# Performance work log

Hardware: AMD Instinct MI355X
Metric: run time of the kernel (lower is better)

## Reference

```python
import jax, jax.numpy as jnp
import numpy as np

B, N, HID, H, M = 4, 16384, 512, 8, 32
D = HID // H  # 64


def setup_inputs() -> dict:
    key = jax.random.key(0)
    ks = jax.random.split(key, 8)
    s = 0.02
    return {
        "x": jax.random.normal(ks[0], (B, N, HID), jnp.float32),
        "wkv": jax.random.normal(ks[1], (2 * HID, HID), jnp.float32) * s,
        "bkv": jnp.zeros((2 * HID,), jnp.float32),
        "wtq": jax.random.normal(ks[2], (H, M, D), jnp.float32) * s,
        "alpha1": jnp.ones((H,), jnp.float32),
        "mix1_w": jax.random.normal(ks[3], (H * M, H * M), jnp.float32) * (1.0 / np.sqrt(H * M)),
        "ln1_w": jnp.ones((D,), jnp.float32),
        "ln1_b": jnp.zeros((D,), jnp.float32),
        "wqkv": jax.random.normal(ks[4], (3 * HID, HID), jnp.float32) * s,
        "wout": jax.random.normal(ks[5], (HID, HID), jnp.float32) * s,
        "bout": jnp.zeros((HID,), jnp.float32),
    }


def _layernorm(x, w, b, eps=1e-5):
    mu = x.mean(-1, keepdims=True)
    var = ((x - mu) ** 2).mean(-1, keepdims=True)
    return (x - mu) * jax.lax.rsqrt(var + eps) * w + b


def reference(x, wkv, bkv, wtq, alpha1, mix1_w, ln1_w, ln1_b, wqkv, wout, bout):
    # key/value projection: [B, N, 2*HID]
    kv = x @ wkv.T + bkv
    xk, xv = jnp.split(kv, 2, axis=-1)
    xk = xk.reshape(B, N, H, D).transpose(0, 2, 1, 3)  # b h n d
    xv = xv.reshape(B, N, H, D).transpose(0, 2, 1, 3)
    # slice scores + 1x1 conv head-mixing over the (H*M) channel dim
    scores = jnp.einsum('hmd,bhnd->bhmn', wtq, xk)
    scores = jnp.einsum('oc,bcn->bon', mix1_w, scores.reshape(B, H * M, N)).reshape(B, H, M, N)
    # softmax over the slice dim M (dim=-2)
    sw = jax.nn.softmax(scores * alpha1[:, None, None], axis=-2)  # b h m n
    # weighted reduction to slice tokens, normalized by total weight per slice
    tok = jnp.einsum('bhmn,bhnd->bhmd', sw, xv)
    tok = tok / (sw.sum(axis=-1, keepdims=True) + 1e-5)
    tok = _layernorm(tok, ln1_w, ln1_b)
    tok = tok.transpose(0, 2, 1, 3).reshape(B, M, HID)  # b m (h d)
    # small inner MHA over the M=32 slice tokens
    qkv = tok @ wqkv.T
    q, k, v = jnp.split(qkv, 3, axis=-1)
    q = q.reshape(B, M, H, D).transpose(0, 2, 1, 3)
    k = k.reshape(B, M, H, D).transpose(0, 2, 1, 3)
    v = v.reshape(B, M, H, D).transpose(0, 2, 1, 3)
    dots = jnp.einsum('bhqd,bhkd->bhqk', q, k) * (D ** -0.5)
    attn = jax.nn.softmax(dots, axis=-1)
    out_tok = jnp.einsum('bhqk,bhkd->bhqd', attn, v)
    # broadcast slice tokens back to the N points via slice weights
    out = jnp.einsum('bhmd,bhmn->bhnd', out_tok, sw)
    out = out.transpose(0, 2, 1, 3).reshape(B, N, HID)
    out = out @ wout.T + bout
    return (out, sw, alpha1[:, None, None], jnp.zeros((H, M), jnp.float32), attn)
```

## Files before the change

### kernel.cpp

```cpp
#include <hip/hip_runtime.h>
#include <hip/hip_bf16.h>

#define B_ 4
#define N_ 16384
#define HID_ 512
#define H_ 8
#define M_ 32
#define D_ 64
#define HM_ 256

typedef __hip_bfloat16 bf16;
typedef __bf16 bf16x8 __attribute__((ext_vector_type(8)));
typedef float f32x4 __attribute__((ext_vector_type(4)));

__device__ __forceinline__ void gl_lds16(const bf16* g, bf16* l) {
    __builtin_amdgcn_global_load_lds(
        (const __attribute__((address_space(1))) void*)g,
        (__attribute__((address_space(3))) void*)l, 16, 0, 0);
}

__device__ __forceinline__ int xcd_swz(int lin, int nwg) {
    return (lin & 7) * (nwg >> 3) + (lin >> 3);
}

__device__ __forceinline__ void stage_tile_lin(const bf16* __restrict__ G, long long r0,
        int kk, int ld, bf16* lds, int t) {
    const int l = t & 63, w = t >> 6;
    const int srow = l >> 3;
    const int skel = (l & 7) * 8;
#pragma unroll
    for (int j = 0; j < 4; ++j) {
        int q = j * 4 + w;
        gl_lds16(G + (r0 + q * 8 + srow) * (long long)ld + kk + skel, lds + q * 512);
    }
}

__device__ __forceinline__ void mfma_core(
        const bf16* __restrict__ Ag, const bf16* __restrict__ Bg,
        long long arow0, int bcol0, int lda, int ldb, int kiters,
        bf16* As, bf16* Bs, f32x4 acc[4][4]) {
    const int t = threadIdx.x;
    const int l = t & 63, w = t >> 6;
    const int wm = w >> 1, wn = w & 1;
    for (int kt = 0; kt < kiters; ++kt) {
        const int kk = kt * 64;
        stage_tile_lin(Ag, arow0, kk, lda, As, t);
        stage_tile_lin(Bg, bcol0, kk, ldb, Bs, t);
        __syncthreads();
#pragma unroll
        for (int ks = 0; ks < 64; ks += 32) {
            bf16x8 af[4], bfr[4];
#pragma unroll
            for (int mf = 0; mf < 4; ++mf)
                af[mf] = *(const bf16x8*)(As + (wm * 64 + mf * 16 + (l & 15)) * 64 + ks + (l >> 4) * 8);
#pragma unroll
            for (int nf = 0; nf < 4; ++nf)
                bfr[nf] = *(const bf16x8*)(Bs + (wn * 64 + nf * 16 + (l & 15)) * 64 + ks + (l >> 4) * 8);
#pragma unroll
            for (int mf = 0; mf < 4; ++mf)
#pragma unroll
                for (int nf = 0; nf < 4; ++nf)
                    acc[mf][nf] = __builtin_amdgcn_mfma_f32_16x16x32_bf16(af[mf], bfr[nf], acc[mf][nf], 0, 0, 0);
        }
        __syncthreads();
    }
}

__global__ __launch_bounds__(256) void k_cast4(const float* __restrict__ s,
        ushort* __restrict__ d) {
    long long i = (long long)blockIdx.x * 256 + threadIdx.x;
    float4 v = reinterpret_cast<const float4*>(s)[i];
    ushort4 o;
    bf16 a0 = __float2bfloat16(v.x), a1 = __float2bfloat16(v.y);
    bf16 a2 = __float2bfloat16(v.z), a3 = __float2bfloat16(v.w);
    o.x = *(ushort*)&a0; o.y = *(ushort*)&a1; o.z = *(ushort*)&a2; o.w = *(ushort*)&a3;
    reinterpret_cast<ushort4*>(d)[i] = o;
}

__global__ __launch_bounds__(256) void k_wfused(const float* __restrict__ mix1,
        const float* __restrict__ wtq, float* __restrict__ wf) {
    const int idx = blockIdx.x * 256 + threadIdx.x;
    const int o = idx >> 9, k = idx & 511;
    const int h = k >> 6, dd = k & 63;
    float s = 0.f;
#pragma unroll
    for (int m = 0; m < 32; ++m)
        s += mix1[(long long)o * 256 + h * 32 + m] * wtq[((long long)h * 32 + m) * 64 + dd];
    wf[(long long)o * 512 + k] = s;
}

__global__ __launch_bounds__(256) void k_wsc(const float* __restrict__ wf,
        const float* __restrict__ wkv, const float* __restrict__ bkv,
        const float* __restrict__ alpha1, bf16* __restrict__ wv_sc,
        float* __restrict__ bias768) {
    __shared__ float wfrow[512];
    __shared__ float red[256];
    const int o = blockIdx.x, t = threadIdx.x;
    wfrow[t] = wf[(long long)o * 512 + t];
    wfrow[t + 256] = wf[(long long)o * 512 + 256 + t];
    __syncthreads();
    const float al = alpha1[o >> 5];
    float a0 = 0.f, a1 = 0.f;
    for (int c = 0; c < 512; ++c) {
        float wv = wfrow[c];
        a0 += wv * wkv[(long long)c * 512 + t];
        a1 += wv * wkv[(long long)c * 512 + t + 256];
    }
    wv_sc[(long long)(512 + o) * 512 + t] = __float2bfloat16(a0 * al);
    wv_sc[(long long)(512 + o) * 512 + t + 256] = __float2bfloat16(a1 * al);
    float p = wfrow[t] * bkv[t] + wfrow[t + 256] * bkv[t + 256];
    red[t] = p; __syncthreads();
    for (int s = 128; s >= 1; s >>= 1) {
        if (t < s) red[t] += red[t + s];
        __syncthreads();
    }
    if (t == 0) bias768[512 + o] = red[0] * al;
}

__global__ __launch_bounds__(256) void k_prep(const float* __restrict__ bkv,
        float* __restrict__ bias768) {
    int j = blockIdx.x * 256 + threadIdx.x;
    bias768[j] = bkv[512 + j];
}

__global__ __launch_bounds__(256) void k12_mfma(const bf16* __restrict__ xb,
        const bf16* __restrict__ wv_sc, const float* __restrict__ bias768,
        bf16* __restrict__ xv, bf16* __restrict__ sc) {
    __shared__ bf16 As[128 * 64], Bs[128 * 64];
    f32x4 acc[4][4];
#pragma unroll
    for (int i = 0; i < 4; ++i)
#pragma unroll
        for (int j = 0; j < 4; ++j) acc[i][j] = (f32x4)(0.0f);
    const int wg = xcd_swz(blockIdx.y * 6 + blockIdx.x, 3072);
    const int bx = wg % 6, by = wg / 6;
    const long long arow0 = (long long)by * 128;
    const int bcol0 = bx * 128;
    mfma_core(xb, wv_sc, arow0, bcol0, 512, 512, 8, As, Bs, acc);
    const int l = threadIdx.x & 63, w = threadIdx.x >> 6;
    const int wm = w >> 1, wn = w & 1;
#pragma unroll
    for (int mf = 0; mf < 4; ++mf) {
#pragma unroll
        for (int nf = 0; nf < 4; ++nf) {
            int col = bcol0 + wn * 64 + nf * 16 + (l & 15);
            float bv = bias768[col];
#pragma unroll
            for (int r = 0; r < 4; ++r) {
                long long row = arow0 + wm * 64 + mf * 16 + (l >> 4) * 4 + r;
                bf16 hv = __float2bfloat16(acc[mf][nf][r] + bv);
                if (col < 512) xv[row * 512 + col] = hv;
                else           sc[row * 256 + (col - 512)] = hv;
            }
        }
    }
}

__global__ __launch_bounds__(256) void k_softmax(const bf16* __restrict__ sc,
        float* __restrict__ swout, bf16* __restrict__ sw_bt,
        float* __restrict__ part) {
    __shared__ float T[32][257];
    const int t = threadIdx.x;
    const int b = blockIdx.y;
    const int n0 = blockIdx.x * 32;
    const long long rb = (long long)b * N_ + n0;
    for (int i = 0; i < 32; ++i)
        T[i][t] = __bfloat162float(sc[(rb + i) * 256 + t]);
    __syncthreads();
    const int nl = t & 31, h = t >> 5;
    float v[32];
    float mx = -1e30f;
#pragma unroll
    for (int i = 0; i < 32; ++i) { v[i] = T[nl][h * 32 + i]; mx = fmaxf(mx, v[i]); }
    float sum = 0.f;
#pragma unroll
    for (int i = 0; i < 32; ++i) { v[i] = __expf(v[i] - mx); sum += v[i]; }
    float rinv = 1.f / sum;
#pragma unroll
    for (int i = 0; i < 32; ++i) T[nl][h * 32 + i] = v[i] * rinv;
    __syncthreads();
#pragma unroll
    for (int jo = 0; jo < 32; ++jo) {
        int o = h * 32 + jo;
        swout[((long long)b * HM_ + o) * N_ + n0 + nl] = T[nl][o];
    }
    for (int i = 0; i < 32; ++i)
        sw_bt[(rb + i) * 256 + t] = __float2bfloat16(T[i][t]);
    float s = 0.f;
#pragma unroll
    for (int i = 0; i < 32; ++i) s += T[i][t];
    part[((long long)b * 512 + blockIdx.x) * 256 + t] = s;
}

__global__ __launch_bounds__(256) void k_swsum2(const float* __restrict__ part,
        float* __restrict__ swsum) {
    const int b = blockIdx.x, c = threadIdx.x;
    float s = 0.f;
    for (int nb = 0; nb < 512; ++nb)
        s += part[((long long)b * 512 + nb) * 256 + c];
    swsum[b * 256 + c] = s;
}

__global__ __launch_bounds__(256) void k3_tok(const float* __restrict__ sw,
        const bf16* __restrict__ xv, float* __restrict__ tok_part) {
    __shared__ __align__(16) float smem[17408];
    float (*swsT)[36] = reinterpret_cast<float(*)[36]>(smem);
    bf16* xvs = reinterpret_cast<bf16*>(smem + 9216);
    const int t = threadIdx.x;
    const int chunk = blockIdx.x;
    const int bh = blockIdx.y;
    const int n0 = chunk * 256;
    const int b = bh >> 3, h = bh & 7;
    const long long swbase = ((long long)bh * 32) * N_ + n0;
#pragma unroll
    for (int p = 0; p < 8; ++p) {
        float4 v;
        v.x = sw[swbase + (long long)(p * 4 + 0) * N_ + t];
        v.y = sw[swbase + (long long)(p * 4 + 1) * N_ + t];
        v.z = sw[swbase + (long long)(p * 4 + 2) * N_ + t];
        v.w = sw[swbase + (long long)(p * 4 + 3) * N_ + t];
        *reinterpret_cast<float4*>(&swsT[t][p * 4]) = v;
    }
    {
        const uint* xg = reinterpret_cast<const uint*>(xv + ((long long)b * N_ + n0) * 512 + h * 64);
        uint* xls = reinterpret_cast<uint*>(xvs);
#pragma unroll
        for (int p = 0; p < 32; ++p) {
            int idx = p * 256 + t;
            int nl = idx >> 5, prt = idx & 31;
            xls[nl * 32 + prt] = xg[(long long)nl * 256 + prt];
        }
    }
    __syncthreads();
    const int l = t & 63, w = t >> 6;
    const int nlh = l >> 5, mtile = (l >> 3) & 3, dtile = l & 7;
    const int m0 = mtile * 8, d0 = dtile * 8;
    float acc[8][8] = {};
    const int wbase = w * 64;
    for (int i = 0; i < 32; ++i) {
        int nl = wbase + i * 2 + nlh;
        float4 s0 = *reinterpret_cast<const float4*>(&swsT[nl][m0]);
        float4 s1 = *reinterpret_cast<const float4*>(&swsT[nl][m0 + 4]);
        uint4 xi = *reinterpret_cast<const uint4*>(&xvs[nl * 64 + d0]);
        float xvf[8];
        xvf[0] = __uint_as_float(xi.x << 16); xvf[1] = __uint_as_float(xi.x & 0xffff0000u);
        xvf[2] = __uint_as_float(xi.y << 16); xvf[3] = __uint_as_float(xi.y & 0xffff0000u);
        xvf[4] = __uint_as_float(xi.z << 16); xvf[5] = __uint_as_float(xi.z & 0xffff0000u);
        xvf[6] = __uint_as_float(xi.w << 16); xvf[7] = __uint_as_float(xi.w & 0xffff0000u);
        float sm[8] = {s0.x, s0.y, s0.z, s0.w, s1.x, s1.y, s1.z, s1.w};
#pragma unroll
        for (int mi = 0; mi < 8; ++mi)
#pragma unroll
            for (int di = 0; di < 8; ++di)
                acc[mi][di] += sm[mi] * xvf[di];
    }
    __syncthreads();
    float* red = smem;
    float* rb = red + (w * 2 + nlh) * 2048;
#pragma unroll
    for (int mi = 0; mi < 8; ++mi) {
        float4 lo = {acc[mi][0], acc[mi][1], acc[mi][2], acc[mi][3]};
        float4 hi = {acc[mi][4], acc[mi][5], acc[mi][6], acc[mi][7]};
        *reinterpret_cast<float4*>(&rb[(m0 + mi) * 64 + d0]) = lo;
        *reinterpret_cast<float4*>(&rb[(m0 + mi) * 64 + d0 + 4]) = hi;
    }
    __syncthreads();
#pragma unroll
    for (int pp = 0; pp < 2; ++pp) {
        int idx4 = pp * 1024 + t * 4;
        float4 s = {0.f, 0.f, 0.f, 0.f};
#pragma unroll
        for (int r = 0; r < 8; ++r) {
            float4 v = *reinterpret_cast<const float4*>(&red[r * 2048 + idx4]);
            s.x += v.x; s.y += v.y; s.z += v.z; s.w += v.w;
        }
        *reinterpret_cast<float4*>(&tok_part[((long long)bh * 64 + chunk) * 2048 + idx4]) = s;
    }
}

__global__ __launch_bounds__(64) void k4a_ln(const float* __restrict__ tok_part,
        const float* __restrict__ swsum, const float* __restrict__ ln_w,
        const float* __restrict__ ln_b, float* __restrict__ tok_ln) {
    const int bid = blockIdx.x;
    const int bh = bid >> 5, m = bid & 31;
    const int d = threadIdx.x;
    float s = 0.f;
    for (int ch = 0; ch < 64; ++ch)
        s += tok_part[(((long long)bh * 64 + ch) * 32 + m) * 64 + d];
    float tokv = s / (swsum[bid] + 1e-5f);
    float mu = tokv;
#pragma unroll
    for (int mk = 32; mk >= 1; mk >>= 1) mu += __shfl_xor(mu, mk, 64);
    mu *= (1.f / 64.f);
    float df = tokv - mu;
    float var = df * df;
#pragma unroll
    for (int mk = 32; mk >= 1; mk >>= 1) var += __shfl_xor(var, mk, 64);
    var *= (1.f / 64.f);
    float y = df * rsqrtf(var + 1e-5f) * ln_w[d] + ln_b[d];
    const int b = bh >> 3, h = bh & 7;
    tok_ln[((long long)b * 32 + m) * 512 + h * 64 + d] = y;
}

__global__ __launch_bounds__(256) void k_wqT(const float* __restrict__ wq,
        float* __restrict__ wqT) {
    __shared__ float tile[32][33];
    const int k0 = blockIdx.x * 32;
    const int j0 = blockIdx.y * 32;
    const int tx = threadIdx.x & 31, ty = threadIdx.x >> 5;
#pragma unroll
    for (int r = 0; r < 32; r += 8)
        tile[ty + r][tx] = wq[(long long)(j0 + ty + r) * 512 + k0 + tx];
    __syncthreads();
#pragma unroll
    for (int r = 0; r < 32; r += 8)
        wqT[(long long)(k0 + ty + r) * 1536 + j0 + tx] = tile[tx][ty + r];
}

__global__ __launch_bounds__(256) void k4b_qkv(const float* __restrict__ tok_ln,
        const float* __restrict__ wqT, float* __restrict__ qkv) {
    const int j = (blockIdx.x % 6) * 256 + threadIdx.x;
    const int r0 = (blockIdx.x / 6) * 4;
    float a0 = 0, a1 = 0, a2 = 0, a3 = 0;
    for (int k = 0; k < 512; ++k) {
        float wv = wqT[(long long)k * 1536 + j];
        a0 += tok_ln[(r0 + 0) * 512 + k] * wv;
        a1 += tok_ln[(r0 + 1) * 512 + k] * wv;
        a2 += tok_ln[(r0 + 2) * 512 + k] * wv;
        a3 += tok_ln[(r0 + 3) * 512 + k] * wv;
    }
    qkv[(long long)(r0 + 0) * 1536 + j] = a0;
    qkv[(long long)(r0 + 1) * 1536 + j] = a1;
    qkv[(long long)(r0 + 2) * 1536 + j] = a2;
    qkv[(long long)(r0 + 3) * 1536 + j] = a3;
}

__global__ __launch_bounds__(256) void k4c_attn(const float* __restrict__ qkv,
        float* __restrict__ out_tok, float* __restrict__ attn_out) {
    __shared__ float qsT[64][33], ksT[64][33], vsT[64][33];
    __shared__ float att[32][33];
    __shared__ float rinv[32];
    const int t = threadIdx.x;
    const int bid = blockIdx.x;
    const int b = bid >> 3, h = bid & 7;
#pragma unroll
    for (int i = 0; i < 8; ++i) {
        int idx = i * 256 + t;
        int mi = idx >> 6, dd = idx & 63;
        long long base = ((long long)b * 32 + mi) * 1536 + h * 64 + dd;
        qsT[dd][mi] = qkv[base];
        ksT[dd][mi] = qkv[base + 512];
        vsT[dd][mi] = qkv[base + 1024];
    }
    __syncthreads();
#pragma unroll
    for (int i = 0; i < 4; ++i) {
        int idx = i * 256 + t;
        int qi = idx >> 5, ki = idx & 31;
        float s = 0.f;
#pragma unroll
        for (int dd = 0; dd < 64; ++dd) s += qsT[dd][qi] * ksT[dd][ki];
        att[qi][ki] = s * 0.125f;
    }
    __syncthreads();
    if (t < 32) {
        float mx = -1e30f;
        for (int k = 0; k < 32; ++k) mx = fmaxf(mx, att[t][k]);
        float sum = 0.f;
        for (int k = 0; k < 32; ++k) { float e = __expf(att[t][k] - mx); att[t][k] = e; sum += e; }
        rinv[t] = 1.f / sum;
    }
    __syncthreads();
#pragma unroll
    for (int i = 0; i < 4; ++i) {
        int idx = i * 256 + t;
        int qi = idx >> 5, ki = idx & 31;
        float a = att[qi][ki] * rinv[qi];
        att[qi][ki] = a;
        attn_out[(long long)bid * 1024 + qi * 32 + ki] = a;
    }
    __syncthreads();
#pragma unroll
    for (int i = 0; i < 8; ++i) {
        int idx = i * 256 + t;
        int qi = idx >> 6, dd = idx & 63;
        float s = 0.f;
#pragma unroll
        for (int ki = 0; ki < 32; ++ki) s += att[qi][ki] * vsT[dd][ki];
        out_tok[((long long)bid * 32 + qi) * 64 + dd] = s;
    }
}

__global__ __launch_bounds__(256) void k5_w2(const float* __restrict__ wout,
        const float* __restrict__ out_tok, bf16* __restrict__ W2) {
    const int bid = blockIdx.x;
    const int b = bid >> 9, o = bid & 511;
    const int t = threadIdx.x;
    const int h = t >> 5, m = t & 31;
    float s = 0.f;
#pragma unroll
    for (int dd = 0; dd < 64; ++dd)
        s += wout[(long long)o * 512 + h * 64 + dd]
           * out_tok[(((long long)b * 8 + h) * 32 + m) * 64 + dd];
    W2[(long long)bid * 256 + t] = __float2bfloat16(s);
}

__global__ __launch_bounds__(256) void k6_mfma(const bf16* __restrict__ sw_bt,
        const bf16* __restrict__ W2, const float* __restrict__ bout,
        float* __restrict__ out) {
    __shared__ bf16 As[128 * 64], Bs[128 * 64];
    f32x4 acc[4][4];
#pragma unroll
    for (int i = 0; i < 4; ++i)
#pragma unroll
        for (int j = 0; j < 4; ++j) acc[i][j] = (f32x4)(0.0f);
    const int wg = xcd_swz((blockIdx.z * 128 + blockIdx.y) * 4 + blockIdx.x, 2048);
    const int bx = wg & 3, by = (wg >> 2) & 127, bz = wg >> 9;
    const long long arow0 = (long long)by * 128;
    const int bcol0 = bx * 128;
    mfma_core(sw_bt + (long long)bz * N_ * 256, W2 + (long long)bz * 512 * 256,
              arow0, bcol0, 256, 256, 4, As, Bs, acc);
    const int l = threadIdx.x & 63, w = threadIdx.x >> 6;
    const int wm = w >> 1, wn = w & 1;
#pragma unroll
    for (int mf = 0; mf < 4; ++mf) {
#pragma unroll
        for (int nf = 0; nf < 4; ++nf) {
            int col = bcol0 + wn * 64 + nf * 16 + (l & 15);
            float bv = bout[col];
#pragma unroll
            for (int r = 0; r < 4; ++r) {
                long long row = arow0 + wm * 64 + mf * 16 + (l >> 4) * 4 + r;
                out[((long long)bz * N_ + row) * 512 + col] = acc[mf][nf][r] + bv;
            }
        }
    }
}

__global__ void k_misc(const float* __restrict__ alpha1,
        float* __restrict__ outA, float* __restrict__ outZ) {
    int t = threadIdx.x;
    if (t < 8) outA[t] = alpha1[t];
    outZ[t] = 0.f;
}

extern "C" void kernel_launch(void* const* d_in, const int* in_sizes, int n_in,
                              void* d_out, int out_size, void* d_ws, size_t ws_size,
                              hipStream_t stream) {
    const float* x      = (const float*)d_in[0];
    const float* wkv    = (const float*)d_in[1];
    const float* bkv    = (const float*)d_in[2];
    const float* wtq    = (const float*)d_in[3];
    const float* alpha1 = (const float*)d_in[4];
    const float* mix1_w = (const float*)d_in[5];
    const float* ln1_w  = (const float*)d_in[6];
    const float* ln1_b  = (const float*)d_in[7];
    const float* wqkv   = (const float*)d_in[8];
    const float* wout   = (const float*)d_in[9];
    const float* bout   = (const float*)d_in[10];

    float* out    = (float*)d_out;
    float* swout  = out + 33554432LL;
    float* alphaO = out + 50331648LL;
    float* zerosO = out + 50331656LL;
    float* attnO  = out + 50331912LL;

    char* ws = (char*)d_ws;
    bf16*  xb        = (bf16*)(ws);
    float* wqkvT     = (float*)(ws);
    float* swsum_prt = (float*)(ws + 33554432LL);
    float* wf_f32    = (float*)(ws + 35651584LL);
    bf16*  sc        = (bf16*)(ws + 67108864LL);
    bf16*  sw_bt     = (bf16*)(ws + 100663296LL);
    bf16*  xv        = (bf16*)(ws + 134217728LL);
    float* tok_part  = (float*)(ws + 201326592LL);
    float* swsum     = (float*)(ws + 218103808LL);
    float* tok_ln    = (float*)(ws + 218107904LL);
    float* qkv       = (float*)(ws + 218370048LL);
    float* out_tok   = (float*)(ws + 219156480LL);
    bf16*  W2b       = (bf16*)(ws + 219418624LL);
    bf16*  wv_sc     = (bf16*)(ws + 220467200LL);
    float* bias768   = (float*)(ws + 221253632LL);

    k_cast4<<<256, 256, 0, stream>>>(wkv + 262144, (ushort*)wv_sc);
    k_wfused<<<512, 256, 0, stream>>>(mix1_w, wtq, wf_f32);
    k_wsc<<<256, 256, 0, stream>>>(wf_f32, wkv, bkv, alpha1, wv_sc, bias768);
    k_prep<<<2, 256, 0, stream>>>(bkv, bias768);
    k_cast4<<<32768, 256, 0, stream>>>(x, (ushort*)xb);
    k12_mfma<<<dim3(6, 512), 256, 0, stream>>>(xb, wv_sc, bias768, xv, sc);
    k_softmax<<<dim3(512, 4), 256, 0, stream>>>(sc, swout, sw_bt, swsum_prt);
    k_wqT<<<dim3(16, 48), 256, 0, stream>>>(wqkv, wqkvT);
    k_swsum2<<<4, 256, 0, stream>>>(swsum_prt, swsum);
    k3_tok<<<dim3(64, 32), 256, 0, stream>>>(swout, xv, tok_part);
    k4a_ln<<<1024, 64, 0, stream>>>(tok_part, swsum, ln1_w, ln1_b, tok_ln);
    k4b_qkv<<<192, 256, 0, stream>>>(tok_ln, wqkvT, qkv);
    k4c_attn<<<32, 256, 0, stream>>>(qkv, out_tok, attnO);
    k5_w2<<<2048, 256, 0, stream>>>(wout, out_tok, W2b);
    k6_mfma<<<dim3(4, 128, 4), 256, 0, stream>>>(sw_bt, W2b, bout, out);
    k_misc<<<1, 256, 0, stream>>>(alpha1, alphaO, zerosO);
}
```

Baseline: 364.1 us.

## Fuse slice softmax and column sums into projection GEMM epilogue

Moves the softmax over the slice dimension into the k12 GEMM epilogue, using wave shuffles across 16-lane groups. It also writes sw (fp32 transposed) and sw_bt (bf16) directly from registers through an LDS staging tile. This removes the bf16 score round-trip through memory and the separate k_softmax and k_swsum2 launches. Per-tile column sums are written as partials and reduced inside k4a_ln, and k3_tok now reads the compact bf16 sw_bt instead of fp32 sw. The softmax epilogue adds register and shuffle work to the GEMM, and k3_tok now uses bf16-rounded weights.

```diff
diff --git a/kernel.cpp b/kernel.cpp
--- a/kernel.cpp
+++ b/kernel.cpp
@@ -21,6 +21,11 @@
 
 __device__ __forceinline__ int xcd_swz(int lin, int nwg) {
     return (lin & 7) * (nwg >> 3) + (lin >> 3);
+}
+
+__device__ __forceinline__ uint bpk(float lo, float hi) {
+    bf16 a = __float2bfloat16(lo), b = __float2bfloat16(hi);
+    return (uint)(*(ushort*)&a) | ((uint)(*(ushort*)&b) << 16);
 }
 
 __device__ __forceinline__ void stage_tile_lin(const bf16* __restrict__ G, long long r0,
@@ -125,8 +130,11 @@
 
 __global__ __launch_bounds__(256) void k12_mfma(const bf16* __restrict__ xb,
         const bf16* __restrict__ wv_sc, const float* __restrict__ bias768,
-        bf16* __restrict__ xv, bf16* __restrict__ sc) {
-    __shared__ bf16 As[128 * 64], Bs[128 * 64];
+        bf16* __restrict__ xv, float* __restrict__ swout,
+        bf16* __restrict__ sw_bt, float* __restrict__ part) {
+    __shared__ __align__(16) bf16 smem[16384];
+    bf16* As = smem;
+    bf16* Bs = smem + 8192;
     f32x4 acc[4][4];
 #pragma unroll
     for (int i = 0; i < 4; ++i)
@@ -137,71 +145,118 @@
     const long long arow0 = (long long)by * 128;
     const int bcol0 = bx * 128;
     mfma_core(xb, wv_sc, arow0, bcol0, 512, 512, 8, As, Bs, acc);
-    const int l = threadIdx.x & 63, w = threadIdx.x >> 6;
-    const int wm = w >> 1, wn = w & 1;
-#pragma unroll
-    for (int mf = 0; mf < 4; ++mf) {
-#pragma unroll
-        for (int nf = 0; nf < 4; ++nf) {
-            int col = bcol0 + wn * 64 + nf * 16 + (l & 15);
-            float bv = bias768[col];
-#pragma unroll
-            for (int r = 0; r < 4; ++r) {
-                long long row = arow0 + wm * 64 + mf * 16 + (l >> 4) * 4 + r;
-                bf16 hv = __float2bfloat16(acc[mf][nf][r] + bv);
-                if (col < 512) xv[row * 512 + col] = hv;
-                else           sc[row * 256 + (col - 512)] = hv;
+
+    const int t = threadIdx.x;
+    const int l = t & 63, w = t >> 6, wm = w >> 1, wn = w & 1;
+    const int l15 = l & 15, lq = l >> 4;
+#pragma unroll
+    for (int nf = 0; nf < 4; ++nf) {
+        float bv = bias768[bcol0 + wn * 64 + nf * 16 + l15];
+#pragma unroll
+        for (int mf = 0; mf < 4; ++mf)
+#pragma unroll
+            for (int r = 0; r < 4; ++r) acc[mf][nf][r] += bv;
+    }
+    float* eps = (float*)smem;
+    float* my = eps + w * 1088;
+
+    if (bcol0 >= 512) {
+#pragma unroll
+        for (int mf = 0; mf < 4; ++mf)
+#pragma unroll
+            for (int r = 0; r < 4; ++r)
+#pragma unroll
+                for (int g = 0; g < 2; ++g) {
+                    float v0 = acc[mf][2 * g][r], v1 = acc[mf][2 * g + 1][r];
+                    float mx = fmaxf(v0, v1);
+#pragma unroll
+                    for (int mk = 1; mk <= 8; mk <<= 1) mx = fmaxf(mx, __shfl_xor(mx, mk));
+                    float e0 = __expf(v0 - mx), e1 = __expf(v1 - mx);
+                    float s = e0 + e1;
+#pragma unroll
+                    for (int mk = 1; mk <= 8; mk <<= 1) s += __shfl_xor(s, mk);
+                    float ri = 1.f / s;
+                    acc[mf][2 * g][r] = e0 * ri;
+                    acc[mf][2 * g + 1][r] = e1 * ri;
+                }
+        {
+            float* cpart = eps + 4352;
+#pragma unroll
+            for (int nf = 0; nf < 4; ++nf) {
+                float ps = 0.f;
+#pragma unroll
+                for (int mf = 0; mf < 4; ++mf)
+#pragma unroll
+                    for (int r = 0; r < 4; ++r) ps += acc[mf][nf][r];
+                ps += __shfl_xor(ps, 16);
+                ps += __shfl_xor(ps, 32);
+                if (lq == 0) cpart[wm * 128 + wn * 64 + nf * 16 + l15] = ps;
             }
-        }
-    }
-}
-
-__global__ __launch_bounds__(256) void k_softmax(const bf16* __restrict__ sc,
-        float* __restrict__ swout, bf16* __restrict__ sw_bt,
-        float* __restrict__ part) {
-    __shared__ float T[32][257];
-    const int t = threadIdx.x;
-    const int b = blockIdx.y;
-    const int n0 = blockIdx.x * 32;
-    const long long rb = (long long)b * N_ + n0;
-    for (int i = 0; i < 32; ++i)
-        T[i][t] = __bfloat162float(sc[(rb + i) * 256 + t]);
-    __syncthreads();
-    const int nl = t & 31, h = t >> 5;
-    float v[32];
-    float mx = -1e30f;
-#pragma unroll
-    for (int i = 0; i < 32; ++i) { v[i] = T[nl][h * 32 + i]; mx = fmaxf(mx, v[i]); }
-    float sum = 0.f;
-#pragma unroll
-    for (int i = 0; i < 32; ++i) { v[i] = __expf(v[i] - mx); sum += v[i]; }
-    float rinv = 1.f / sum;
-#pragma unroll
-    for (int i = 0; i < 32; ++i) T[nl][h * 32 + i] = v[i] * rinv;
-    __syncthreads();
-#pragma unroll
-    for (int jo = 0; jo < 32; ++jo) {
-        int o = h * 32 + jo;
-        swout[((long long)b * HM_ + o) * N_ + n0 + nl] = T[nl][o];
-    }
-    for (int i = 0; i < 32; ++i)
-        sw_bt[(rb + i) * 256 + t] = __float2bfloat16(T[i][t]);
-    float s = 0.f;
-#pragma unroll
-    for (int i = 0; i < 32; ++i) s += T[i][t];
-    part[((long long)b * 512 + blockIdx.x) * 256 + t] = s;
-}
-
-__global__ __launch_bounds__(256) void k_swsum2(const float* __restrict__ part,
-        float* __restrict__ swsum) {
-    const int b = blockIdx.x, c = threadIdx.x;
-    float s = 0.f;
-    for (int nb = 0; nb < 512; ++nb)
-        s += part[((long long)b * 512 + nb) * 256 + c];
-    swsum[b * 256 + c] = s;
-}
-
-__global__ __launch_bounds__(256) void k3_tok(const float* __restrict__ sw,
+            __syncthreads();
+            if (t < 128)
+                part[(long long)by * 256 + (bcol0 - 512) + t] = cpart[t] + cpart[128 + t];
+            __syncthreads();
+        }
+        const int b = (int)(arow0 >> 14);
+        const int nloc = (int)(arow0 & 16383) + wm * 64;
+#pragma unroll
+        for (int mf = 0; mf < 4; ++mf) {
+#pragma unroll
+            for (int nf = 0; nf < 4; ++nf)
+#pragma unroll
+                for (int r = 0; r < 4; ++r)
+                    my[(lq * 4 + r) * 68 + nf * 16 + l15] = acc[mf][nf][r];
+#pragma unroll
+            for (int p = 0; p < 2; ++p) {
+                int lrow = p * 8 + (l >> 3);
+                const float* src = my + lrow * 68 + (l & 7) * 8;
+                float4 v0 = *(const float4*)src, v1 = *(const float4*)(src + 4);
+                uint4 pk;
+                pk.x = bpk(v0.x, v0.y); pk.y = bpk(v0.z, v0.w);
+                pk.z = bpk(v1.x, v1.y); pk.w = bpk(v1.z, v1.w);
+                long long grow = arow0 + wm * 64 + mf * 16 + lrow;
+                int gcol = (bcol0 - 512) + wn * 64 + (l & 7) * 8;
+                *reinterpret_cast<uint4*>(sw_bt + grow * 256 + gcol) = pk;
+            }
+            {
+                int cglob = (bcol0 - 512) + wn * 64 + l;
+                float* dst = swout + ((long long)b * HM_ + cglob) * N_ + nloc + mf * 16;
+#pragma unroll
+                for (int r4 = 0; r4 < 4; ++r4) {
+                    float4 v;
+                    v.x = my[(r4 * 4 + 0) * 68 + l];
+                    v.y = my[(r4 * 4 + 1) * 68 + l];
+                    v.z = my[(r4 * 4 + 2) * 68 + l];
+                    v.w = my[(r4 * 4 + 3) * 68 + l];
+                    *reinterpret_cast<float4*>(dst + r4 * 4) = v;
+                }
+            }
+        }
+    } else {
+#pragma unroll
+        for (int mf = 0; mf < 4; ++mf) {
+#pragma unroll
+            for (int nf = 0; nf < 4; ++nf)
+#pragma unroll
+                for (int r = 0; r < 4; ++r)
+                    my[(lq * 4 + r) * 68 + nf * 16 + l15] = acc[mf][nf][r];
+#pragma unroll
+            for (int p = 0; p < 2; ++p) {
+                int lrow = p * 8 + (l >> 3);
+                const float* src = my + lrow * 68 + (l & 7) * 8;
+                float4 v0 = *(const float4*)src, v1 = *(const float4*)(src + 4);
+                uint4 pk;
+                pk.x = bpk(v0.x, v0.y); pk.y = bpk(v0.z, v0.w);
+                pk.z = bpk(v1.x, v1.y); pk.w = bpk(v1.z, v1.w);
+                long long grow = arow0 + wm * 64 + mf * 16 + lrow;
+                int gcol = bcol0 + wn * 64 + (l & 7) * 8;
+                *reinterpret_cast<uint4*>(xv + grow * 512 + gcol) = pk;
+            }
+        }
+    }
+}
+
+__global__ __launch_bounds__(256) void k3_tok(const bf16* __restrict__ sw_bt,
         const bf16* __restrict__ xv, float* __restrict__ tok_part) {
     __shared__ __align__(16) float smem[17408];
     float (*swsT)[36] = reinterpret_cast<float(*)[36]>(smem);
@@ -211,15 +266,17 @@
     const int bh = blockIdx.y;
     const int n0 = chunk * 256;
     const int b = bh >> 3, h = bh & 7;
-    const long long swbase = ((long long)bh * 32) * N_ + n0;
-#pragma unroll
-    for (int p = 0; p < 8; ++p) {
-        float4 v;
-        v.x = sw[swbase + (long long)(p * 4 + 0) * N_ + t];
-        v.y = sw[swbase + (long long)(p * 4 + 1) * N_ + t];
-        v.z = sw[swbase + (long long)(p * 4 + 2) * N_ + t];
-        v.w = sw[swbase + (long long)(p * 4 + 3) * N_ + t];
-        *reinterpret_cast<float4*>(&swsT[t][p * 4]) = v;
+    {
+        const long long base = ((long long)(b * N_ + n0 + t)) * 256 + h * 32;
+        const uint4* sp = reinterpret_cast<const uint4*>(sw_bt + base);
+        uint4 qs[4] = {sp[0], sp[1], sp[2], sp[3]};
+        const uint* qu = reinterpret_cast<const uint*>(qs);
+#pragma unroll
+        for (int j = 0; j < 16; ++j) {
+            uint u = qu[j];
+            swsT[t][2 * j] = __uint_as_float(u << 16);
+            swsT[t][2 * j + 1] = __uint_as_float(u & 0xffff0000u);
+        }
     }
     {
         const uint* xg = reinterpret_cast<const uint*>(xv + ((long long)b * N_ + n0) * 512 + h * 64);
@@ -279,7 +336,7 @@
 }
 
 __global__ __launch_bounds__(64) void k4a_ln(const float* __restrict__ tok_part,
-        const float* __restrict__ swsum, const float* __restrict__ ln_w,
+        const float* __restrict__ part, const float* __restrict__ ln_w,
         const float* __restrict__ ln_b, float* __restrict__ tok_ln) {
     const int bid = blockIdx.x;
     const int bh = bid >> 5, m = bid & 31;
@@ -287,7 +344,12 @@
     float s = 0.f;
     for (int ch = 0; ch < 64; ++ch)
         s += tok_part[(((long long)bh * 64 + ch) * 32 + m) * 64 + d];
-    float tokv = s / (swsum[bid] + 1e-5f);
+    const int b = bid >> 8, c = bid & 255;
+    float ssum = part[((long long)(b * 128 + d)) * 256 + c]
+               + part[((long long)(b * 128 + 64 + d)) * 256 + c];
+#pragma unroll
+    for (int mk = 32; mk >= 1; mk >>= 1) ssum += __shfl_xor(ssum, mk, 64);
+    float tokv = s / (ssum + 1e-5f);
     float mu = tokv;
 #pragma unroll
     for (int mk = 32; mk >= 1; mk >>= 1) mu += __shfl_xor(mu, mk, 64);
@@ -298,8 +360,8 @@
     for (int mk = 32; mk >= 1; mk >>= 1) var += __shfl_xor(var, mk, 64);
     var *= (1.f / 64.f);
     float y = df * rsqrtf(var + 1e-5f) * ln_w[d] + ln_b[d];
-    const int b = bh >> 3, h = bh & 7;
-    tok_ln[((long long)b * 32 + m) * 512 + h * 64 + d] = y;
+    const int bb = bh >> 3, h = bh & 7;
+    tok_ln[((long long)bb * 32 + m) * 512 + h * 64 + d] = y;
 }
 
 __global__ __launch_bounds__(256) void k_wqT(const float* __restrict__ wq,
@@ -468,13 +530,11 @@
     char* ws = (char*)d_ws;
     bf16*  xb        = (bf16*)(ws);
     float* wqkvT     = (float*)(ws);
-    float* swsum_prt = (float*)(ws + 33554432LL);
     float* wf_f32    = (float*)(ws + 35651584LL);
-    bf16*  sc        = (bf16*)(ws + 67108864LL);
+    float* part      = (float*)(ws + 67108864LL);
     bf16*  sw_bt     = (bf16*)(ws + 100663296LL);
     bf16*  xv        = (bf16*)(ws + 134217728LL);
     float* tok_part  = (float*)(ws + 201326592LL);
-    float* swsum     = (float*)(ws + 218103808LL);
     float* tok_ln    = (float*)(ws + 218107904LL);
     float* qkv       = (float*)(ws + 218370048LL);
     float* out_tok   = (float*)(ws + 219156480LL);
@@ -487,12 +547,10 @@
     k_wsc<<<256, 256, 0, stream>>>(wf_f32, wkv, bkv, alpha1, wv_sc, bias768);
     k_prep<<<2, 256, 0, stream>>>(bkv, bias768);
     k_cast4<<<32768, 256, 0, stream>>>(x, (ushort*)xb);
-    k12_mfma<<<dim3(6, 512), 256, 0, stream>>>(xb, wv_sc, bias768, xv, sc);
-    k_softmax<<<dim3(512, 4), 256, 0, stream>>>(sc, swout, sw_bt, swsum_prt);
+    k12_mfma<<<dim3(6, 512), 256, 0, stream>>>(xb, wv_sc, bias768, xv, swout, sw_bt, part);
     k_wqT<<<dim3(16, 48), 256, 0, stream>>>(wqkv, wqkvT);
-    k_swsum2<<<4, 256, 0, stream>>>(swsum_prt, swsum);
-    k3_tok<<<dim3(64, 32), 256, 0, stream>>>(swout, xv, tok_part);
-    k4a_ln<<<1024, 64, 0, stream>>>(tok_part, swsum, ln1_w, ln1_b, tok_ln);
+    k3_tok<<<dim3(64, 32), 256, 0, stream>>>(sw_bt, xv, tok_part);
+    k4a_ln<<<1024, 64, 0, stream>>>(tok_part, part, ln1_w, ln1_b, tok_ln);
     k4b_qkv<<<192, 256, 0, stream>>>(tok_ln, wqkvT, qkv);
     k4c_attn<<<32, 256, 0, stream>>>(qkv, out_tok, attnO);
     k5_w2<<<2048, 256, 0, stream>>>(wout, out_tok, W2b);
```

Measured after the change: 362.2 us. Within noise of the previous version (-0.5%).
